# Optimization experiments

Hardware: AMD Instinct MI355X
Metric: run time of the kernel (lower is better)

The kernel has to match this reference:

```python
import jax, jax.numpy as jnp
import numpy as np

N, EMB, CHEB_K, H, DIN = 512, 10, 2, 64, 2
LSTM_H = 130


def _avwgcn(x, S_base, mask_t, node_emb, W_pool, b_pool):
    # x: [B,N,C], S_base: [N,N] softmax(relu(E E^T)), mask_t: [B,N,N]
    B = x.shape[0]
    S = S_base[None, :, :] * mask_t                      # [B,N,N]
    eye = jnp.broadcast_to(jnp.eye(N, dtype=x.dtype), (B, N, N))
    supports = [eye, S]
    for _ in range(2, CHEB_K):
        supports.append(2.0 * jnp.matmul(S, supports[-1]) - supports[-2])
    sup = jnp.stack(supports, axis=0)                    # [K,B,N,N]
    weights = jnp.einsum('nd,dkio->nkio', node_emb, W_pool)   # [N,K,I,O]
    bias = node_emb @ b_pool                             # [N,O]
    x_g = jnp.einsum('kbnm,bmc->bnkc', sup, x)           # [B,N,K,C]
    return jnp.einsum('bnki,nkio->bno', x_g, weights) + bias


def _encoder(entity, entity_mask, node_emb, gW, gb, uW, ub):
    # entity: [B,T,N,DIN]; returns last hidden state [B,N,H]
    B = entity.shape[0]
    S_base = jax.nn.softmax(jax.nn.relu(node_emb @ node_emb.T), axis=-1)
    x_seq = jnp.swapaxes(entity, 0, 1)                   # [T,B,N,DIN]
    m_seq = jnp.swapaxes(entity_mask, 0, 1)              # [T,B,N,N]

    def step(state, xm):
        x_t, m_t = xm
        ins = jnp.concatenate([x_t, state], axis=-1)     # [B,N,DIN+H]
        z_r = jax.nn.sigmoid(_avwgcn(ins, S_base, m_t, node_emb, gW, gb))
        z, r = z_r[..., :H], z_r[..., H:]
        cand = jnp.concatenate([x_t, z * state], axis=-1)
        hc = jnp.tanh(_avwgcn(cand, S_base, m_t, node_emb, uW, ub))
        h = r * state + (1.0 - r) * hc
        return h, None

    state0 = jnp.zeros((B, N, H), dtype=entity.dtype)
    state, _ = jax.lax.scan(step, state0, (x_seq, m_seq))
    return state                                         # [B,N,H]


def _lstm_layer(x_seq, Wih, Whh, bih, bhh):
    # x_seq: [T,B,in]; PyTorch gate order i,f,g,o
    B = x_seq.shape[1]
    Hh = LSTM_H

    def step(carry, xt):
        h, c = carry
        g = xt @ Wih.T + h @ Whh.T + bih + bhh           # [B,4H]
        i = jax.nn.sigmoid(g[:, :Hh])
        f = jax.nn.sigmoid(g[:, Hh:2 * Hh])
        gg = jnp.tanh(g[:, 2 * Hh:3 * Hh])
        o = jax.nn.sigmoid(g[:, 3 * Hh:])
        c = f * c + i * gg
        h = o * jnp.tanh(c)
        return (h, c), h

    init = (jnp.zeros((B, Hh), x_seq.dtype), jnp.zeros((B, Hh), x_seq.dtype))
    (_, _), hs = jax.lax.scan(step, init, x_seq)
    return hs                                            # [T,B,H]


def setup_inputs() -> dict:
    key = jax.random.key(0)
    ks = jax.random.split(key, 20)
    s = 0.1
    inp = {
        'entity': jax.random.normal(ks[0], (16, 12, N, DIN), jnp.float32),
        'entity_mask': jnp.ones((16, 12, N, N), jnp.float32),
        's_and_r': jax.random.normal(ks[1], (16, 32, 64), jnp.float32),
        'node_emb': jax.random.normal(ks[2], (N, EMB), jnp.float32),
        'gW': jax.random.normal(ks[3], (EMB, CHEB_K, DIN + H, 2 * H), jnp.float32) * s,
        'gb': jax.random.normal(ks[4], (EMB, 2 * H), jnp.float32) * s,
        'uW': jax.random.normal(ks[5], (EMB, CHEB_K, DIN + H, H), jnp.float32) * s,
        'ub': jax.random.normal(ks[6], (EMB, H), jnp.float32) * s,
        'lstm_Wih0': jax.random.normal(ks[7], (4 * LSTM_H, 64), jnp.float32) * s,
        'lstm_Whh0': jax.random.normal(ks[8], (4 * LSTM_H, LSTM_H), jnp.float32) * s,
        'lstm_bih0': jax.random.normal(ks[9], (4 * LSTM_H,), jnp.float32) * s,
        'lstm_bhh0': jax.random.normal(ks[10], (4 * LSTM_H,), jnp.float32) * s,
        'lstm_Wih1': jax.random.normal(ks[11], (4 * LSTM_H, LSTM_H), jnp.float32) * s,
        'lstm_Whh1': jax.random.normal(ks[12], (4 * LSTM_H, LSTM_H), jnp.float32) * s,
        'lstm_bih1': jax.random.normal(ks[13], (4 * LSTM_H,), jnp.float32) * s,
        'lstm_bhh1': jax.random.normal(ks[14], (4 * LSTM_H,), jnp.float32) * s,
        'fc_W': jax.random.normal(ks[15], (24, LSTM_H + H), jnp.float32) * s,
        'fc_b': jax.random.normal(ks[16], (24,), jnp.float32) * s,
    }
    return inp


def reference(entity, entity_mask, s_and_r, node_emb, gW, gb, uW, ub,
              lstm_Wih0, lstm_Whh0, lstm_bih0, lstm_bhh0,
              lstm_Wih1, lstm_Whh1, lstm_bih1, lstm_bhh1, fc_W, fc_b):
    B = entity.shape[0]
    # graph encoder: last hidden state, max over nodes
    h_graph = _encoder(entity, entity_mask, node_emb, gW, gb, uW, ub)  # [B,N,H]
    graph_out = jnp.max(h_graph, axis=1)                               # [B,H]
    # 2-layer LSTM (eval mode, dropout inactive)
    x_seq = jnp.swapaxes(s_and_r, 0, 1)                 # [T,B,in]
    h1 = _lstm_layer(x_seq, lstm_Wih0, lstm_Whh0, lstm_bih0, lstm_bhh0)
    h2 = _lstm_layer(h1, lstm_Wih1, lstm_Whh1, lstm_bih1, lstm_bhh1)
    sr_out = h2[-1]                                      # [B,130]
    feat = jnp.concatenate([sr_out, graph_out], axis=-1)
    out = jax.nn.sigmoid(feat @ fc_W.T + fc_b)           # [B,24]
    return out.reshape(B, 12, 2)
```

## Files before the change

### kernel.cpp

```cpp
#include <hip/hip_runtime.h>
#include <math.h>

#define NN 512
#define EMBD 10
#define HH 64
#define DINV 2
#define CIN 66
#define TT 12
#define BB 16
#define LH 130
#define LG 520
#define PART ((size_t)BB * NN * CIN)

typedef __attribute__((ext_vector_type(8))) short short8;
typedef __attribute__((ext_vector_type(8))) _Float16 half8;
typedef __attribute__((ext_vector_type(4))) float f32x4;
typedef __attribute__((ext_vector_type(2))) _Float16 h2v;

__device__ __forceinline__ float sigmoidf_(float x) { return 1.f / (1.f + __expf(-x)); }
__device__ __forceinline__ float tanhf_(float x)    { return 1.f - 2.f / (1.f + __expf(2.f * x)); }
__device__ __forceinline__ unsigned short f16u_(float v) {
    return __builtin_bit_cast(unsigned short, (_Float16)v);
}
__device__ __forceinline__ unsigned pkh_(float a, float b) {
    return (unsigned)f16u_(a) | ((unsigned)f16u_(b) << 16);
}
__device__ __forceinline__ float fdot2_(unsigned h, unsigned w, float c) {
#if __has_builtin(__builtin_amdgcn_fdot2)
    return __builtin_amdgcn_fdot2(__builtin_bit_cast(h2v, h), __builtin_bit_cast(h2v, w), c, false);
#else
    h2v H = __builtin_bit_cast(h2v, h), W = __builtin_bit_cast(h2v, w);
    return c + (float)H[0] * (float)W[0] + (float)H[1] * (float)W[1];
#endif
}
__device__ __forceinline__ float plo_(unsigned u) { return (float)__builtin_bit_cast(h2v, u)[0]; }
__device__ __forceinline__ float phi_(unsigned u) { return (float)__builtin_bit_cast(h2v, u)[1]; }
__device__ __forceinline__ half8 ld8h_(const unsigned short* p) {
    return __builtin_bit_cast(half8, *(const short8*)p);
}

__global__ __launch_bounds__(256) void precompute1_kernel(
    const float* __restrict__ emb, float* __restrict__ Sb,
    const float* __restrict__ gW, const float* __restrict__ uW,
    unsigned short* __restrict__ WgF, unsigned short* __restrict__ WuF,
    const float* __restrict__ gb, const float* __restrict__ ub,
    float* __restrict__ bgc, float* __restrict__ buc,
    const float* __restrict__ Wih0, const float* __restrict__ Whh0,
    const float* __restrict__ Wih1, const float* __restrict__ Whh1,
    unsigned* __restrict__ wp_ih0, unsigned* __restrict__ wp_hh0,
    unsigned* __restrict__ wp_ih1, unsigned* __restrict__ wp_hh1) {
    __shared__ float poolS[EMBD * 512];
    __shared__ float embS[128 * EMBD];
    __shared__ float redw[4];
    const int bid = blockIdx.x;
    const int tid = threadIdx.x;
    if (bid < 512) {
        const int n = bid;
        float* en = embS;
        if (tid < EMBD) en[tid] = emb[n * EMBD + tid];
        __syncthreads();
        float v[2];
        #pragma unroll
        for (int q = 0; q < 2; q++) {
            int m = tid + q * 256;
            float s = 0.f;
            #pragma unroll
            for (int d = 0; d < EMBD; d++) s += en[d] * emb[m * EMBD + d];
            v[q] = fmaxf(s, 0.f);
        }
        float mx = fmaxf(v[0], v[1]);
        for (int off = 32; off >= 1; off >>= 1) mx = fmaxf(mx, __shfl_xor(mx, off));
        if ((tid & 63) == 0) redw[tid >> 6] = mx;
        __syncthreads();
        mx = fmaxf(fmaxf(redw[0], redw[1]), fmaxf(redw[2], redw[3]));
        __syncthreads();
        v[0] = __expf(v[0] - mx);
        v[1] = __expf(v[1] - mx);
        float sm = v[0] + v[1];
        for (int off = 32; off >= 1; off >>= 1) sm += __shfl_xor(sm, off);
        if ((tid & 63) == 0) redw[tid >> 6] = sm;
        __syncthreads();
        sm = redw[0] + redw[1] + redw[2] + redw[3];
        float inv = 1.f / sm;
        Sb[n * NN + tid]       = v[0] * inv;
        Sb[n * NN + tid + 256] = v[1] * inv;
        return;
    }
    if (bid < 752) {
        const int bb = bid - 512;
        const int group = bb % 60;
        const int chunk = bb / 60;
        const float* pool;
        unsigned short* outU;
        int OT, Ow, ot, kc;
        if (group < 40) { pool = gW; outU = WgF; Ow = 128; OT = 8; ot = group / 5; kc = group % 5; }
        else { int g2 = group - 40; pool = uW; outU = WuF; Ow = 64; OT = 4; ot = g2 / 5; kc = g2 % 5; }
        for (int l = tid; l < EMBD * 512; l += 256) {
            int d = l >> 9, rem = l & 511;
            int kpl = rem >> 4, ol = rem & 15;
            int kp = kc * 32 + kpl;
            float v = 0.f;
            if (kp < 2 * CIN) v = pool[((size_t)d * (2 * CIN) + kp) * Ow + ot * 16 + ol];
            poolS[l] = v;
        }
        for (int l = tid; l < 128 * EMBD; l += 256) {
            int nl = l / EMBD, d = l - nl * EMBD;
            embS[l] = emb[(chunk * 128 + nl) * EMBD + d];
        }
        __syncthreads();
        const int e0 = tid * 2, e1 = e0 + 1;
        const int l0 = e0 >> 3, j0 = e0 & 7, p0 = (((l0 >> 4) << 3) + j0) * 16 + (l0 & 15);
        const int l1 = e1 >> 3, j1 = e1 & 7, p1 = (((l1 >> 4) << 3) + j1) * 16 + (l1 & 15);
        float w0[EMBD], w1[EMBD];
        #pragma unroll
        for (int d = 0; d < EMBD; d++) {
            w0[d] = poolS[d * 512 + p0];
            w1[d] = poolS[d * 512 + p1];
        }
        for (int nl = 0; nl < 128; nl++) {
            int n = chunk * 128 + nl;
            float a0 = 0.f, a1 = 0.f;
            #pragma unroll
            for (int d = 0; d < EMBD; d++) {
                float e = embS[nl * EMBD + d];
                a0 += e * w0[d];
                a1 += e * w1[d];
            }
            size_t base = (((size_t)n * OT + ot) * 5 + kc) * 512;
            *(unsigned*)(outU + base + e0) = pkh_(a0, a1);
        }
        return;
    }
    if (bid < 1136) {
        int idx = (bid - 752) * 256 + tid;
        if (idx < NN * 128) {
            int n = idx >> 7, rem = idx & 127;
            float a = 0.f;
            #pragma unroll
            for (int d = 0; d < EMBD; d++) a += emb[n * EMBD + d] * gb[d * 128 + rem];
            bgc[idx] = a;
        } else if (idx < NN * 128 + NN * 64) {
            int j = idx - NN * 128;
            int n = j >> 6, rem = j & 63;
            float a = 0.f;
            #pragma unroll
            for (int d = 0; d < EMBD; d++) a += emb[n * EMBD + d] * ub[d * 64 + rem];
            buc[j] = a;
        }
        return;
    }
    {
        int idx = (bid - 1136) * 256 + tid;
        const float* w;
        unsigned* wp;
        int K, base;
        if (idx < 16640)       { w = Wih0; wp = wp_ih0; K = 64;  base = 0; }
        else if (idx < 50440)  { w = Whh0; wp = wp_hh0; K = 130; base = 16640; }
        else if (idx < 84240)  { w = Wih1; wp = wp_ih1; K = 130; base = 50440; }
        else if (idx < 118040) { w = Whh1; wp = wp_hh1; K = 130; base = 84240; }
        else return;
        int j2 = idx - base;
        int kk = j2 / LG, j = j2 - kk * LG;
        wp[j2] = pkh_(w[j * K + 2 * kk], w[j * K + 2 * kk + 1]);
    }
}

__device__ void lstm_body(int b, int tid,
    const float* __restrict__ sr,
    const unsigned* __restrict__ wp_ih0, const float* __restrict__ Wih0,
    const float* __restrict__ bih0, const float* __restrict__ bhh0,
    const unsigned* __restrict__ wp_hh0, const float* __restrict__ Whh0,
    const unsigned* __restrict__ wp_ih1, const float* __restrict__ Wih1,
    const float* __restrict__ bih1, const float* __restrict__ bhh1,
    const unsigned* __restrict__ wp_hh1, const float* __restrict__ Whh1,
    float* __restrict__ h2last) {
    const int lane = tid & 63;
    const int wv = tid >> 6;
    __shared__ __align__(16) float xp[32 * 520];
    __shared__ __align__(16) unsigned h1p[32 * 68];
    __shared__ __align__(16) float h1s[32 * 132];
    __shared__ __align__(16) unsigned xsp[32 * 32];
    __shared__ __align__(16) unsigned hP[68];
    __shared__ __align__(16) float hS[132], cS[132];
    __shared__ float gS[520];
    __shared__ float WeX[130 * 8];
    unsigned wpk[65];

    for (int l = tid; l < 32 * 32; l += 512) {
        float2 v = *(const float2*)&sr[(size_t)b * 2048 + 2 * l];
        xsp[l] = pkh_(v.x, v.y);
    }
    #pragma unroll
    for (int kk = 0; kk < 32; kk++) wpk[kk] = wp_ih0[kk * 520 + tid];
    for (int l = tid; l < 64 * 8; l += 512) { int k = l >> 3, je = l & 7; WeX[l] = Wih0[(512 + je) * 64 + k]; }
    __syncthreads();
    {
        float bias = bih0[tid] + bhh0[tid];
        for (int t = 0; t < 32; t++) {
            const uint4* x4 = (const uint4*)&xsp[t * 32];
            float a0 = bias, a1 = 0.f;
            #pragma unroll
            for (int q = 0; q < 8; q++) {
                uint4 hq = x4[q];
                a0 = fdot2_(hq.x, wpk[4 * q + 0], a0);
                a1 = fdot2_(hq.y, wpk[4 * q + 1], a1);
                a0 = fdot2_(hq.z, wpk[4 * q + 2], a0);
                a1 = fdot2_(hq.w, wpk[4 * q + 3], a1);
            }
            xp[t * 520 + tid] = a0 + a1;
        }
        if (tid < 256) {
            int je = tid & 7, t = tid >> 3;
            float a = bih0[512 + je] + bhh0[512 + je];
            for (int p = 0; p < 32; p++) {
                unsigned u = xsp[t * 32 + p];
                a += plo_(u) * WeX[(2 * p) * 8 + je] + phi_(u) * WeX[(2 * p + 1) * 8 + je];
            }
            xp[t * 520 + 512 + je] = a;
        }
    }
    __syncthreads();

    #pragma unroll
    for (int kk = 0; kk < 65; kk++) wpk[kk] = wp_hh0[kk * 520 + tid];
    for (int l = tid; l < 130 * 8; l += 512) { int k = l >> 3, je = l & 7; WeX[l] = Whh0[(512 + je) * 130 + k]; }
    for (int l = tid; l < 132; l += 512) { hS[l] = 0.f; cS[l] = 0.f; }
    if (tid < 68) hP[tid] = 0u;
    __syncthreads();
    {
        float we0 = WeX[lane * 8 + wv];
        float we1 = WeX[(lane + 64) * 8 + wv];
        float we2 = (lane < 2) ? WeX[(lane + 128) * 8 + wv] : 0.f;
        for (int t = 0; t < 32; t++) {
            const uint4* hp4 = (const uint4*)hP;
            float a0 = xp[t * 520 + tid], a1 = 0.f;
            #pragma unroll
            for (int q = 0; q < 16; q++) {
                uint4 hq = hp4[q];
                a0 = fdot2_(hq.x, wpk[4 * q + 0], a0);
                a1 = fdot2_(hq.y, wpk[4 * q + 1], a1);
                a0 = fdot2_(hq.z, wpk[4 * q + 2], a0);
                a1 = fdot2_(hq.w, wpk[4 * q + 3], a1);
            }
            a0 = fdot2_(hP[64], wpk[64], a0);
            gS[tid] = a0 + a1;
            float p = hS[lane] * we0 + hS[lane + 64] * we1;
            if (lane < 2) p += hS[lane + 128] * we2;
            #pragma unroll
            for (int off = 32; off >= 1; off >>= 1) p += __shfl_xor(p, off);
            if (lane == 0) gS[512 + wv] = xp[t * 520 + 512 + wv] + p;
            __syncthreads();
            if (tid < 130) {
                float iv = sigmoidf_(gS[tid]);
                float fv = sigmoidf_(gS[130 + tid]);
                float gv = tanhf_(gS[260 + tid]);
                float ov = sigmoidf_(gS[390 + tid]);
                float cv = fv * cS[tid] + iv * gv;
                cS[tid] = cv;
                float hv = ov * tanhf_(cv);
                hS[tid] = hv;
                h1s[t * 132 + tid] = hv;
                float nb = __shfl_xor(hv, 1);
                if ((tid & 1) == 0) {
                    unsigned pk = pkh_(hv, nb);
                    hP[tid >> 1] = pk;
                    h1p[t * 68 + (tid >> 1)] = pk;
                }
            }
            __syncthreads();
        }
    }

    #pragma unroll
    for (int kk = 0; kk < 65; kk++) wpk[kk] = wp_ih1[kk * 520 + tid];
    for (int l = tid; l < 130 * 8; l += 512) { int k = l >> 3, je = l & 7; WeX[l] = Wih1[(512 + je) * 130 + k]; }
    __syncthreads();
    {
        float bias = bih1[tid] + bhh1[tid];
        for (int t = 0; t < 32; t++) {
            const uint4* x4 = (const uint4*)&h1p[t * 68];
            float a0 = bias, a1 = 0.f;
            #pragma unroll
            for (int q = 0; q < 16; q++) {
                uint4 hq = x4[q];
                a0 = fdot2_(hq.x, wpk[4 * q + 0], a0);
                a1 = fdot2_(hq.y, wpk[4 * q + 1], a1);
                a0 = fdot2_(hq.z, wpk[4 * q + 2], a0);
                a1 = fdot2_(hq.w, wpk[4 * q + 3], a1);
            }
            a0 = fdot2_(h1p[t * 68 + 64], wpk[64], a0);
            xp[t * 520 + tid] = a0 + a1;
        }
        if (tid < 256) {
            int je = tid & 7, t = tid >> 3;
            float a = bih1[512 + je] + bhh1[512 + je];
            for (int k = 0; k < 130; k++) a += h1s[t * 132 + k] * WeX[k * 8 + je];
            xp[t * 520 + 512 + je] = a;
        }
    }
    __syncthreads();

    #pragma unroll
    for (int kk = 0; kk < 65; kk++) wpk[kk] = wp_hh1[kk * 520 + tid];
    for (int l = tid; l < 130 * 8; l += 512) { int k = l >> 3, je = l & 7; WeX[l] = Whh1[(512 + je) * 130 + k]; }
    for (int l = tid; l < 132; l += 512) { hS[l] = 0.f; cS[l] = 0.f; }
    if (tid < 68) hP[tid] = 0u;
    __syncthreads();
    {
        float we0 = WeX[lane * 8 + wv];
        float we1 = WeX[(lane + 64) * 8 + wv];
        float we2 = (lane < 2) ? WeX[(lane + 128) * 8 + wv] : 0.f;
        for (int t = 0; t < 32; t++) {
            const uint4* hp4 = (const uint4*)hP;
            float a0 = xp[t * 520 + tid], a1 = 0.f;
            #pragma unroll
            for (int q = 0; q < 16; q++) {
                uint4 hq = hp4[q];
                a0 = fdot2_(hq.x, wpk[4 * q + 0], a0);
                a1 = fdot2_(hq.y, wpk[4 * q + 1], a1);
                a0 = fdot2_(hq.z, wpk[4 * q + 2], a0);
                a1 = fdot2_(hq.w, wpk[4 * q + 3], a1);
            }
            a0 = fdot2_(hP[64], wpk[64], a0);
            gS[tid] = a0 + a1;
            float p = hS[lane] * we0 + hS[lane + 64] * we1;
            if (lane < 2) p += hS[lane + 128] * we2;
            #pragma unroll
            for (int off = 32; off >= 1; off >>= 1) p += __shfl_xor(p, off);
            if (lane == 0) gS[512 + wv] = xp[t * 520 + 512 + wv] + p;
            __syncthreads();
            if (tid < 130) {
                float iv = sigmoidf_(gS[tid]);
                float fv = sigmoidf_(gS[130 + tid]);
                float gv = tanhf_(gS[260 + tid]);
                float ov = sigmoidf_(gS[390 + tid]);
                float cv = fv * cS[tid] + iv * gv;
                cS[tid] = cv;
                float hv = ov * tanhf_(cv);
                hS[tid] = hv;
                float nb = __shfl_xor(hv, 1);
                if ((tid & 1) == 0) hP[tid >> 1] = pkh_(hv, nb);
                if (t == 31) h2last[(size_t)b * LH + tid] = hv;
            }
            __syncthreads();
        }
    }
}

__global__ __launch_bounds__(512) void mega_kernel(
    const float* __restrict__ Sb, const float* __restrict__ mask,
    unsigned short* __restrict__ AF,
    const float* __restrict__ ent, unsigned short* __restrict__ Xf,
    float* __restrict__ state,
    const float* __restrict__ sr,
    const unsigned* __restrict__ wp_ih0, const float* __restrict__ Wih0,
    const float* __restrict__ bih0, const float* __restrict__ bhh0,
    const unsigned* __restrict__ wp_hh0, const float* __restrict__ Whh0,
    const unsigned* __restrict__ wp_ih1, const float* __restrict__ Wih1,
    const float* __restrict__ bih1, const float* __restrict__ bhh1,
    const unsigned* __restrict__ wp_hh1, const float* __restrict__ Whh1,
    float* __restrict__ h2last) {
    const int bid = blockIdx.x;
    const int tid = threadIdx.x;
    if (bid < 16) {
        lstm_body(bid, tid, sr, wp_ih0, Wih0, bih0, bhh0, wp_hh0, Whh0,
                  wp_ih1, Wih1, bih1, bhh1, wp_hh1, Whh1, h2last);
        return;
    }
    if (bid < 176) {
        int idx = (bid - 16) * 512 + tid;
        int l = idx & 63;
        int r = idx >> 6;
        int kc = r & 1; r >>= 1;
        int ct = r % 5; r /= 5;
        int q = r & 7;
        int b = r >> 3;
        const int c = ct * 16 + (l & 15);
        const int mbase = q * 64 + kc * 32 + ((l >> 4) & 3) * 8;
        union { unsigned short u[8]; short8 v; } o;
        #pragma unroll
        for (int j = 0; j < 8; j++) {
            int m = mbase + j;
            float v = 0.f;
            if (c < DINV) v = ent[((size_t)(b * TT + 0) * NN + m) * DINV + c];
            o.u[j] = f16u_(v);
        }
        size_t base = ((((size_t)b * 8 + q) * 5 + ct) * 2 + kc) * 512;
        *(short8*)(Xf + base + l * 8) = o.v;
        return;
    }
    if (bid < 1200) {
        int i = (bid - 176) * 512 + tid;
        state[i] = 0.f;
        return;
    }
    size_t idx = (size_t)(bid - 1200) * 512 + tid;
    int l = (int)(idx & 63);
    size_t f = idx >> 6;
    int mch = (int)(f & 15); f >>= 4;
    int ntile = (int)(f & 31); f >>= 5;
    int t = (int)(f % 12);
    int b = (int)(f / 12);
    int nrow = ntile * 16 + (l & 15);
    int m0 = mch * 32 + ((l >> 4) & 3) * 8;
    const float4* s4 = (const float4*)(Sb + (size_t)nrow * NN + m0);
    const float4* m4 = (const float4*)(mask + ((size_t)(b * TT + t) * NN + nrow) * NN + m0);
    float4 sa = s4[0], sc = s4[1];
    float4 ma = m4[0], mc = m4[1];
    union { unsigned short u[8]; short8 v; } o;
    o.u[0] = f16u_(sa.x * ma.x); o.u[1] = f16u_(sa.y * ma.y);
    o.u[2] = f16u_(sa.z * ma.z); o.u[3] = f16u_(sa.w * ma.w);
    o.u[4] = f16u_(sc.x * mc.x); o.u[5] = f16u_(sc.y * mc.y);
    o.u[6] = f16u_(sc.z * mc.z); o.u[7] = f16u_(sc.w * mc.w);
    *(short8*)(AF + idx * 8) = o.v;
}

__global__ __launch_bounds__(256) void spmm_kernel(const unsigned short* __restrict__ AF,
                                                   const unsigned short* __restrict__ Xf,
                                                   float* __restrict__ out, int t) {
    const int tid = threadIdx.x;
    const int lane = tid & 63;
    const int w = tid >> 6;
    const int b = blockIdx.y;
    const int z = blockIdx.z;
    float* __restrict__ outp = out + (size_t)z * PART;
    const int ntile = blockIdx.x * 4 + w;

    f32x4 acc[5];
    #pragma unroll
    for (int ct = 0; ct < 5; ct++) acc[ct] = (f32x4){0.f, 0.f, 0.f, 0.f};

    #pragma unroll
    for (int r2 = 0; r2 < 2; r2++) {
        #pragma unroll
        for (int kc = 0; kc < 2; kc++) {
            const int mch = z * 4 + r2 * 2 + kc;
            const int q = z * 2 + r2;
            half8 a = ld8h_(AF + ((((size_t)b * TT + t) * 32 + ntile) * 16 + mch) * 512 + lane * 8);
            #pragma unroll
            for (int ct = 0; ct < 5; ct++) {
                half8 bf = ld8h_(Xf + ((((size_t)b * 8 + q) * 5 + ct) * 2 + kc) * 512 + lane * 8);
                acc[ct] = __builtin_amdgcn_mfma_f32_16x16x32_f16(a, bf, acc[ct], 0, 0, 0);
            }
        }
    }
    const int col = lane & 15, rq = lane >> 4;
    #pragma unroll
    for (int ct = 0; ct < 5; ct++) {
        int c = ct * 16 + col;
        if (c < CIN) {
            #pragma unroll
            for (int reg = 0; reg < 4; reg++) {
                int n = ntile * 16 + rq * 4 + reg;
                outp[(size_t)b * NN * CIN + n * CIN + c] = acc[ct][reg];
            }
        }
    }
}

__global__ __launch_bounds__(256) void gate_mfma_kernel(const float* __restrict__ ent,
                                                        const float* __restrict__ state,
                                                        const float* __restrict__ xg1,
                                                        const unsigned short* __restrict__ WgF,
                                                        const float* __restrict__ bg,
                                                        float* __restrict__ cand,
                                                        float* __restrict__ rbuf,
                                                        unsigned short* __restrict__ Xf,
                                                        int t) {
    __shared__ unsigned short A_h[16 * 168];
    const int n = blockIdx.x;
    const int tid = threadIdx.x;
    const int lane = tid & 63;
    const int w = tid >> 6;
    for (int idx = tid; idx < 16 * 36; idx += 256) {
        int b = idx / 36, k = 132 + idx - b * 36;
        A_h[b * 168 + k] = 0;
    }
    for (int idx = tid; idx < 16 * 132; idx += 256) {
        int b = idx / 132, ip = idx - b * 132;
        float v;
        if (ip < CIN) {
            v = (ip < DINV) ? ent[((size_t)(b * TT + t) * NN + n) * DINV + ip]
                            : state[((size_t)b * NN + n) * HH + (ip - DINV)];
        } else {
            size_t g = (size_t)b * NN * CIN + n * CIN + (ip - CIN);
            v = xg1[g] + xg1[g + PART] + xg1[g + 2 * PART] + xg1[g + 3 * PART];
        }
        A_h[b * 168 + ip] = f16u_(v);
    }
    __syncthreads();

    f32x4 acc0 = {0.f, 0.f, 0.f, 0.f}, acc1 = {0.f, 0.f, 0.f, 0.f};
    const unsigned short* Wn = WgF + (size_t)n * (8 * 5 * 512);
    #pragma unroll
    for (int kc = 0; kc < 5; kc++) {
        int aoff = (lane & 15) * 168 + kc * 32 + (lane >> 4) * 8;
        half8 ah = ld8h_(&A_h[aoff]);
        half8 bh0 = ld8h_(Wn + ((size_t)(w * 5) + kc) * 512 + lane * 8);
        half8 bh1 = ld8h_(Wn + ((size_t)((w + 4) * 5) + kc) * 512 + lane * 8);
        acc0 = __builtin_amdgcn_mfma_f32_16x16x32_f16(ah, bh0, acc0, 0, 0, 0);
        acc1 = __builtin_amdgcn_mfma_f32_16x16x32_f16(ah, bh1, acc1, 0, 0, 0);
    }
    const int col = lane & 15, rq = lane >> 4;
    const int q = n >> 6, kcn = (n >> 5) & 1, jn = n & 7;
    {
        int o = w * 16 + col;
        int c = o + DINV;
        int ct = c >> 4, cl = c & 15;
        int l = ((n >> 3) & 3) * 16 + cl;
        float bias = bg[n * 128 + o];
        #pragma unroll
        for (int reg = 0; reg < 4; reg++) {
            int b = rq * 4 + reg;
            float zr = sigmoidf_(acc0[reg] + bias);
            float val = zr * state[((size_t)b * NN + n) * HH + o];
            cand[(size_t)b * NN * CIN + n * CIN + c] = val;
            size_t fb = ((((size_t)b * 8 + q) * 5 + ct) * 2 + kcn) * 512;
            Xf[fb + l * 8 + jn] = f16u_(val);
        }
    }
    {
        int o = (w + 4) * 16 + col;
        float bias = bg[n * 128 + o];
        #pragma unroll
        for (int reg = 0; reg < 4; reg++) {
            int b = rq * 4 + reg;
            float zr = sigmoidf_(acc1[reg] + bias);
            rbuf[((size_t)b * NN + n) * HH + (o - HH)] = zr;
        }
    }
    if (tid < 32) {
        int b = tid >> 1, i = tid & 1;
        cand[(size_t)b * NN * CIN + n * CIN + i] =
            ent[((size_t)(b * TT + t) * NN + n) * DINV + i];
    }
}

__global__ __launch_bounds__(256) void update_mfma_kernel(const float* __restrict__ cand,
                                                          const float* __restrict__ xg2,
                                                          const unsigned short* __restrict__ WuF,
                                                          const float* __restrict__ bu,
                                                          const float* __restrict__ rbuf,
                                                          float* __restrict__ state,
                                                          unsigned short* __restrict__ Xf,
                                                          const float* __restrict__ ent,
                                                          int tnext) {
    __shared__ unsigned short A_h[16 * 168];
    const int n = blockIdx.x;
    const int tid = threadIdx.x;
    const int lane = tid & 63;
    const int w = tid >> 6;
    for (int idx = tid; idx < 16 * 36; idx += 256) {
        int b = idx / 36, k = 132 + idx - b * 36;
        A_h[b * 168 + k] = 0;
    }
    for (int idx = tid; idx < 16 * 132; idx += 256) {
        int b = idx / 132, ip = idx - b * 132;
        float v;
        if (ip < CIN) {
            v = cand[(size_t)b * NN * CIN + n * CIN + ip];
        } else {
            size_t g = (size_t)b * NN * CIN + n * CIN + (ip - CIN);
            v = xg2[g] + xg2[g + PART] + xg2[g + 2 * PART] + xg2[g + 3 * PART];
        }
        A_h[b * 168 + ip] = f16u_(v);
    }
    __syncthreads();

    f32x4 acc = {0.f, 0.f, 0.f, 0.f};
    const unsigned short* Wn = WuF + (size_t)n * (4 * 5 * 512);
    #pragma unroll
    for (int kc = 0; kc < 5; kc++) {
        int aoff = (lane & 15) * 168 + kc * 32 + (lane >> 4) * 8;
        half8 ah = ld8h_(&A_h[aoff]);
        half8 bh = ld8h_(Wn + ((size_t)(w * 5) + kc) * 512 + lane * 8);
        acc = __builtin_amdgcn_mfma_f32_16x16x32_f16(ah, bh, acc, 0, 0, 0);
    }
    const int col = lane & 15, rq = lane >> 4;
    const int q = n >> 6, kcn = (n >> 5) & 1, jn = n & 7;
    int o = w * 16 + col;
    int c = o + DINV;
    int ct = c >> 4, cl = c & 15;
    int l = ((n >> 3) & 3) * 16 + cl;
    float bias = bu[n * HH + o];
    #pragma unroll
    for (int reg = 0; reg < 4; reg++) {
        int b = rq * 4 + reg;
        float hc = tanhf_(acc[reg] + bias);
        size_t g = ((size_t)b * NN + n) * HH + o;
        float rr = rbuf[g];
        float ns = rr * state[g] + (1.f - rr) * hc;
        state[g] = ns;
        size_t fb = ((((size_t)b * 8 + q) * 5 + ct) * 2 + kcn) * 512;
        Xf[fb + l * 8 + jn] = f16u_(ns);
    }
    if (w == 0 && col < DINV && tnext < TT) {
        int le = ((n >> 3) & 3) * 16 + col;
        #pragma unroll
        for (int reg = 0; reg < 4; reg++) {
            int b = rq * 4 + reg;
            float v = ent[((size_t)(b * TT + tnext) * NN + n) * DINV + col];
            size_t fb = ((((size_t)b * 8 + q) * 5 + 0) * 2 + kcn) * 512;
            Xf[fb + le * 8 + jn] = f16u_(v);
        }
    }
}

__global__ __launch_bounds__(256) void final_kernel(const float* __restrict__ state,
                                                    const float* __restrict__ h2last,
                                                    const float* __restrict__ fcW,
                                                    const float* __restrict__ fcb,
                                                    float* __restrict__ out) {
    const int b = blockIdx.x;
    const int tid = threadIdx.x;
    __shared__ float feat[LH + HH];
    __shared__ float red[4][HH];
    const int hh = tid & 63, q = tid >> 6;
    float mx = -INFINITY;
    for (int n = q * 128; n < q * 128 + 128; n++)
        mx = fmaxf(mx, state[((size_t)b * NN + n) * HH + hh]);
    red[q][hh] = mx;
    if (tid >= 64 && tid < 64 + LH)
        feat[tid - 64] = h2last[(size_t)b * LH + (tid - 64)];
    __syncthreads();
    if (tid < HH)
        feat[LH + tid] = fmaxf(fmaxf(red[0][tid], red[1][tid]), fmaxf(red[2][tid], red[3][tid]));
    __syncthreads();
    if (tid < 24) {
        float a = fcb[tid];
        for (int k = 0; k < LH + HH; k++) a += feat[k] * fcW[tid * (LH + HH) + k];
        out[b * 24 + tid] = sigmoidf_(a);
    }
}

extern "C" void kernel_launch(void* const* d_in, const int* in_sizes, int n_in,
                              void* d_out, int out_size, void* d_ws, size_t ws_size,
                              hipStream_t stream) {
    const float* ent  = (const float*)d_in[0];
    const float* mask = (const float*)d_in[1];
    const float* sr   = (const float*)d_in[2];
    const float* emb  = (const float*)d_in[3];
    const float* gW   = (const float*)d_in[4];
    const float* gb   = (const float*)d_in[5];
    const float* uW   = (const float*)d_in[6];
    const float* ub   = (const float*)d_in[7];
    const float* Wih0 = (const float*)d_in[8];
    const float* Whh0 = (const float*)d_in[9];
    const float* bih0 = (const float*)d_in[10];
    const float* bhh0 = (const float*)d_in[11];
    const float* Wih1 = (const float*)d_in[12];
    const float* Whh1 = (const float*)d_in[13];
    const float* bih1 = (const float*)d_in[14];
    const float* bhh1 = (const float*)d_in[15];
    const float* fcW  = (const float*)d_in[16];
    const float* fcb  = (const float*)d_in[17];
    float* out = (float*)d_out;
    float* ws = (float*)d_ws;

    size_t off = 0;
    float* Sb     = ws + off; off += (size_t)NN * NN;
    unsigned short* WgF = (unsigned short*)(ws + off); off += (size_t)NN * 8 * 5 * 256;
    unsigned short* WuF = (unsigned short*)(ws + off); off += (size_t)NN * 4 * 5 * 256;
    unsigned short* AF  = (unsigned short*)(ws + off); off += (size_t)BB * TT * 32 * 16 * 256;
    float* bgc    = ws + off; off += (size_t)NN * 128;
    float* buc    = ws + off; off += (size_t)NN * HH;
    float* state  = ws + off; off += (size_t)BB * NN * HH;
    float* xgP    = ws + off; off += 4 * PART;
    float* cand   = ws + off; off += PART;
    float* rbuf   = ws + off; off += (size_t)BB * NN * HH;
    float* h2last = ws + off; off += (size_t)BB * LH;
    unsigned short* Xf = (unsigned short*)(ws + off); off += (size_t)BB * 8 * 5 * 2 * 256;
    unsigned* wp_ih0 = (unsigned*)(ws + off); off += 32 * LG;
    unsigned* wp_hh0 = (unsigned*)(ws + off); off += 65 * LG;
    unsigned* wp_ih1 = (unsigned*)(ws + off); off += 65 * LG;
    unsigned* wp_hh1 = (unsigned*)(ws + off); off += 65 * LG;

    precompute1_kernel<<<1598, 256, 0, stream>>>(emb, Sb, gW, uW, WgF, WuF, gb, ub, bgc, buc,
                                                 Wih0, Whh0, Wih1, Whh1,
                                                 wp_ih0, wp_hh0, wp_ih1, wp_hh1);
    mega_kernel<<<13488, 512, 0, stream>>>(Sb, mask, AF, ent, Xf, state, sr,
                                           wp_ih0, Wih0, bih0, bhh0, wp_hh0, Whh0,
                                           wp_ih1, Wih1, bih1, bhh1, wp_hh1, Whh1, h2last);

    for (int t = 0; t < TT; t++) {
        spmm_kernel<<<dim3(8, BB, 4), 256, 0, stream>>>(AF, Xf, xgP, t);
        gate_mfma_kernel<<<NN, 256, 0, stream>>>(ent, state, xgP, WgF, bgc, cand, rbuf, Xf, t);
        spmm_kernel<<<dim3(8, BB, 4), 256, 0, stream>>>(AF, Xf, xgP, t);
        update_mfma_kernel<<<NN, 256, 0, stream>>>(cand, xgP, WuF, buc, rbuf, state, Xf, ent, t + 1);
    }

    final_kernel<<<BB, 256, 0, stream>>>(state, h2last, fcW, fcb, out);
}
```

Measured before the change: 643.2 us.

## Interleave LSTM recurrent gate rows so each quad computes its cell update

```diff
diff --git a/kernel.cpp b/kernel.cpp
--- a/kernel.cpp
+++ b/kernel.cpp
@@ -153,15 +153,20 @@
         int idx = (bid - 1136) * 256 + tid;
         const float* w;
         unsigned* wp;
-        int K, base;
-        if (idx < 16640)       { w = Wih0; wp = wp_ih0; K = 64;  base = 0; }
-        else if (idx < 50440)  { w = Whh0; wp = wp_hh0; K = 130; base = 16640; }
-        else if (idx < 84240)  { w = Wih1; wp = wp_ih1; K = 130; base = 50440; }
-        else if (idx < 118040) { w = Whh1; wp = wp_hh1; K = 130; base = 84240; }
+        int K, base, hh;
+        if (idx < 16640)       { w = Wih0; wp = wp_ih0; K = 64;  base = 0;     hh = 0; }
+        else if (idx < 50440)  { w = Whh0; wp = wp_hh0; K = 130; base = 16640; hh = 1; }
+        else if (idx < 84240)  { w = Wih1; wp = wp_ih1; K = 130; base = 50440; hh = 0; }
+        else if (idx < 118040) { w = Whh1; wp = wp_hh1; K = 130; base = 84240; hh = 1; }
         else return;
         int j2 = idx - base;
         int kk = j2 / LG, j = j2 - kk * LG;
-        wp[j2] = pkh_(w[j * K + 2 * kk], w[j * K + 2 * kk + 1]);
+        int dst = j;
+        if (hh) {
+            int u = j % 130, gg = j / 130;
+            dst = (u < 128) ? (u * 4 + gg) : (512 + (u - 128) * 4 + gg);
+        }
+        wp[kk * LG + dst] = pkh_(w[j * K + 2 * kk], w[j * K + 2 * kk + 1]);
     }
 }
 
@@ -174,17 +179,17 @@
     const float* __restrict__ bih1, const float* __restrict__ bhh1,
     const unsigned* __restrict__ wp_hh1, const float* __restrict__ Whh1,
     float* __restrict__ h2last) {
-    const int lane = tid & 63;
-    const int wv = tid >> 6;
     __shared__ __align__(16) float xp[32 * 520];
-    __shared__ __align__(16) unsigned h1p[32 * 68];
-    __shared__ __align__(16) float h1s[32 * 132];
+    __shared__ __align__(16) unsigned short h1ph[32 * 136];
     __shared__ __align__(16) unsigned xsp[32 * 32];
-    __shared__ __align__(16) unsigned hP[68];
-    __shared__ __align__(16) float hS[132], cS[132];
-    __shared__ float gS[520];
+    __shared__ __align__(16) unsigned short hPh[2][136];
+    __shared__ __align__(16) unsigned WeH[8 * 66];
     __shared__ float WeX[130 * 8];
     unsigned wpk[65];
+    const int g = tid & 3, ju = tid >> 2;
+    const int xrow = g * 130 + ju;
+    const int lw = tid & 63;
+    const bool w0 = (tid < 64);
 
     for (int l = tid; l < 32 * 32; l += 512) {
         float2 v = *(const float2*)&sr[(size_t)b * 2048 + 2 * l];
@@ -223,48 +228,69 @@
 
     #pragma unroll
     for (int kk = 0; kk < 65; kk++) wpk[kk] = wp_hh0[kk * 520 + tid];
-    for (int l = tid; l < 130 * 8; l += 512) { int k = l >> 3, je = l & 7; WeX[l] = Whh0[(512 + je) * 130 + k]; }
-    for (int l = tid; l < 132; l += 512) { hS[l] = 0.f; cS[l] = 0.f; }
-    if (tid < 68) hP[tid] = 0u;
+    for (int l = tid; l < 8 * 65; l += 512) {
+        int rw = l / 65, kp = l - rw * 65;
+        WeH[rw * 66 + kp] = wp_hh0[kp * 520 + 512 + rw];
+    }
+    for (int l = tid; l < 2 * 136; l += 512) ((unsigned short*)hPh)[l] = 0;
     __syncthreads();
     {
-        float we0 = WeX[lane * 8 + wv];
-        float we1 = WeX[(lane + 64) * 8 + wv];
-        float we2 = (lane < 2) ? WeX[(lane + 128) * 8 + wv] : 0.f;
+        float creg = 0.f, cx = 0.f;
         for (int t = 0; t < 32; t++) {
-            const uint4* hp4 = (const uint4*)hP;
-            float a0 = xp[t * 520 + tid], a1 = 0.f;
+            const unsigned short* hc = hPh[t & 1];
+            unsigned short* hn = hPh[(t + 1) & 1];
+            const uint4* h4 = (const uint4*)hc;
+            float a0 = xp[t * 520 + xrow], a1 = 0.f;
             #pragma unroll
             for (int q = 0; q < 16; q++) {
-                uint4 hq = hp4[q];
+                uint4 hq = h4[q];
                 a0 = fdot2_(hq.x, wpk[4 * q + 0], a0);
                 a1 = fdot2_(hq.y, wpk[4 * q + 1], a1);
                 a0 = fdot2_(hq.z, wpk[4 * q + 2], a0);
                 a1 = fdot2_(hq.w, wpk[4 * q + 3], a1);
             }
-            a0 = fdot2_(hP[64], wpk[64], a0);
-            gS[tid] = a0 + a1;
-            float p = hS[lane] * we0 + hS[lane + 64] * we1;
-            if (lane < 2) p += hS[lane + 128] * we2;
-            #pragma unroll
-            for (int off = 32; off >= 1; off >>= 1) p += __shfl_xor(p, off);
-            if (lane == 0) gS[512 + wv] = xp[t * 520 + 512 + wv] + p;
-            __syncthreads();
-            if (tid < 130) {
-                float iv = sigmoidf_(gS[tid]);
-                float fv = sigmoidf_(gS[130 + tid]);
-                float gv = tanhf_(gS[260 + tid]);
-                float ov = sigmoidf_(gS[390 + tid]);
-                float cv = fv * cS[tid] + iv * gv;
-                cS[tid] = cv;
-                float hv = ov * tanhf_(cv);
-                hS[tid] = hv;
-                h1s[t * 132 + tid] = hv;
-                float nb = __shfl_xor(hv, 1);
-                if ((tid & 1) == 0) {
-                    unsigned pk = pkh_(hv, nb);
-                    hP[tid >> 1] = pk;
-                    h1p[t * 68 + (tid >> 1)] = pk;
+            a0 = fdot2_(*(const unsigned*)(hc + 128), wpk[64], a0);
+            float p = a0 + a1;
+            float p1 = __shfl_xor(p, 1);
+            float p2 = __shfl_xor(p, 2);
+            float p3 = __shfl_xor(p1, 2);
+            float ip = (g == 0) ? p : (g == 1) ? p1 : (g == 2) ? p2 : p3;
+            float fp = (g == 1) ? p : (g == 0) ? p1 : (g == 3) ? p2 : p3;
+            float gp = (g == 2) ? p : (g == 3) ? p1 : (g == 0) ? p2 : p3;
+            float op = (g == 3) ? p : (g == 2) ? p1 : (g == 1) ? p2 : p3;
+            float iv = sigmoidf_(ip), fv = sigmoidf_(fp), gv = tanhf_(gp), ov = sigmoidf_(op);
+            float cv = fv * creg + iv * gv;
+            creg = cv;
+            float hv = ov * tanhf_(cv);
+            if (g == 0) {
+                unsigned short hu = f16u_(hv);
+                hn[ju] = hu;
+                h1ph[t * 136 + ju] = hu;
+            }
+            if (w0) {
+                int rw = lw >> 3;
+                float e0 = 0.f;
+                for (int kp = (lw & 7); kp < 65; kp += 8)
+                    e0 = fdot2_(*(const unsigned*)(hc + 2 * kp), WeH[rw * 66 + kp], e0);
+                e0 += __shfl_xor(e0, 1);
+                e0 += __shfl_xor(e0, 2);
+                e0 += __shfl_xor(e0, 4);
+                int er = (rw & 3) * 130 + 128 + (rw >> 2);
+                float pe = e0 + xp[t * 520 + er];
+                int bl = lw & 32;
+                float pi_ = __shfl(pe, bl);
+                float pf_ = __shfl(pe, bl + 8);
+                float pg_ = __shfl(pe, bl + 16);
+                float po_ = __shfl(pe, bl + 24);
+                if ((lw & 31) == 0) {
+                    float iv2 = sigmoidf_(pi_), fv2 = sigmoidf_(pf_), gv2 = tanhf_(pg_), ov2 = sigmoidf_(po_);
+                    float cv2 = fv2 * cx + iv2 * gv2;
+                    cx = cv2;
+                    float hv2 = ov2 * tanhf_(cv2);
+                    int uu = 128 + (lw >> 5);
+                    unsigned short hu2 = f16u_(hv2);
+                    hn[uu] = hu2;
+                    h1ph[t * 136 + uu] = hu2;
                 }
             }
             __syncthreads();
@@ -278,7 +304,7 @@
     {
         float bias = bih1[tid] + bhh1[tid];
         for (int t = 0; t < 32; t++) {
-            const uint4* x4 = (const uint4*)&h1p[t * 68];
+            const uint4* x4 = (const uint4*)&h1ph[t * 136];
             float a0 = bias, a1 = 0.f;
             #pragma unroll
             for (int q = 0; q < 16; q++) {
@@ -288,13 +314,16 @@
                 a0 = fdot2_(hq.z, wpk[4 * q + 2], a0);
                 a1 = fdot2_(hq.w, wpk[4 * q + 3], a1);
             }
-            a0 = fdot2_(h1p[t * 68 + 64], wpk[64], a0);
+            a0 = fdot2_(*(const unsigned*)&h1ph[t * 136 + 128], wpk[64], a0);
             xp[t * 520 + tid] = a0 + a1;
         }
         if (tid < 256) {
             int je = tid & 7, t = tid >> 3;
             float a = bih1[512 + je] + bhh1[512 + je];
-            for (int k = 0; k < 130; k++) a += h1s[t * 132 + k] * WeX[k * 8 + je];
+            for (int k = 0; k < 65; k++) {
+                unsigned u = *(const unsigned*)&h1ph[t * 136 + 2 * k];
+                a += plo_(u) * WeX[(2 * k) * 8 + je] + phi_(u) * WeX[(2 * k + 1) * 8 + je];
+            }
             xp[t * 520 + 512 + je] = a;
         }
     }
@@ -302,45 +331,68 @@
 
     #pragma unroll
     for (int kk = 0; kk < 65; kk++) wpk[kk] = wp_hh1[kk * 520 + tid];
-    for (int l = tid; l < 130 * 8; l += 512) { int k = l >> 3, je = l & 7; WeX[l] = Whh1[(512 + je) * 130 + k]; }
-    for (int l = tid; l < 132; l += 512) { hS[l] = 0.f; cS[l] = 0.f; }
-    if (tid < 68) hP[tid] = 0u;
+    for (int l = tid; l < 8 * 65; l += 512) {
+        int rw = l / 65, kp = l - rw * 65;
+        WeH[rw * 66 + kp] = wp_hh1[kp * 520 + 512 + rw];
+    }
+    for (int l = tid; l < 2 * 136; l += 512) ((unsigned short*)hPh)[l] = 0;
     __syncthreads();
     {
-        float we0 = WeX[lane * 8 + wv];
-        float we1 = WeX[(lane + 64) * 8 + wv];
-        float we2 = (lane < 2) ? WeX[(lane + 128) * 8 + wv] : 0.f;
+        float creg = 0.f, cx = 0.f;
         for (int t = 0; t < 32; t++) {
-            const uint4* hp4 = (const uint4*)hP;
-            float a0 = xp[t * 520 + tid], a1 = 0.f;
+            const unsigned short* hc = hPh[t & 1];
+            unsigned short* hn = hPh[(t + 1) & 1];
+            const uint4* h4 = (const uint4*)hc;
+            float a0 = xp[t * 520 + xrow], a1 = 0.f;
             #pragma unroll
             for (int q = 0; q < 16; q++) {
-                uint4 hq = hp4[q];
+                uint4 hq = h4[q];
                 a0 = fdot2_(hq.x, wpk[4 * q + 0], a0);
                 a1 = fdot2_(hq.y, wpk[4 * q + 1], a1);
                 a0 = fdot2_(hq.z, wpk[4 * q + 2], a0);
                 a1 = fdot2_(hq.w, wpk[4 * q + 3], a1);
             }
-            a0 = fdot2_(hP[64], wpk[64], a0);
-            gS[tid] = a0 + a1;
-            float p = hS[lane] * we0 + hS[lane + 64] * we1;
-            if (lane < 2) p += hS[lane + 128] * we2;
-            #pragma unroll
-            for (int off = 32; off >= 1; off >>= 1) p += __shfl_xor(p, off);
-            if (lane == 0) gS[512 + wv] = xp[t * 520 + 512 + wv] + p;
-            __syncthreads();
-            if (tid < 130) {
-                float iv = sigmoidf_(gS[tid]);
-                float fv = sigmoidf_(gS[130 + tid]);
-                float gv = tanhf_(gS[260 + tid]);
-                float ov = sigmoidf_(gS[390 + tid]);
-                float cv = fv * cS[tid] + iv * gv;
-                cS[tid] = cv;
-                float hv = ov * tanhf_(cv);
-                hS[tid] = hv;
-                float nb = __shfl_xor(hv, 1);
-                if ((tid & 1) == 0) hP[tid >> 1] = pkh_(hv, nb);
-                if (t == 31) h2last[(size_t)b * LH + tid] = hv;
+            a0 = fdot2_(*(const unsigned*)(hc + 128), wpk[64], a0);
+            float p = a0 + a1;
+            float p1 = __shfl_xor(p, 1);
+            float p2 = __shfl_xor(p, 2);
+            float p3 = __shfl_xor(p1, 2);
+            float ip = (g == 0) ? p : (g == 1) ? p1 : (g == 2) ? p2 : p3;
+            float fp = (g == 1) ? p : (g == 0) ? p1 : (g == 3) ? p2 : p3;
+            float gp = (g == 2) ? p : (g == 3) ? p1 : (g == 0) ? p2 : p3;
+            float op = (g == 3) ? p : (g == 2) ? p1 : (g == 1) ? p2 : p3;
+            float iv = sigmoidf_(ip), fv = sigmoidf_(fp), gv = tanhf_(gp), ov = sigmoidf_(op);
+            float cv = fv * creg + iv * gv;
+            creg = cv;
+            float hv = ov * tanhf_(cv);
+            if (g == 0) {
+                hn[ju] = f16u_(hv);
+                if (t == 31) h2last[(size_t)b * LH + ju] = hv;
+            }
+            if (w0) {
+                int rw = lw >> 3;
+                float e0 = 0.f;
+                for (int kp = (lw & 7); kp < 65; kp += 8)
+                    e0 = fdot2_(*(const unsigned*)(hc + 2 * kp), WeH[rw * 66 + kp], e0);
+                e0 += __shfl_xor(e0, 1);
+                e0 += __shfl_xor(e0, 2);
+                e0 += __shfl_xor(e0, 4);
+                int er = (rw & 3) * 130 + 128 + (rw >> 2);
+                float pe = e0 + xp[t * 520 + er];
+                int bl = lw & 32;
+                float pi_ = __shfl(pe, bl);
+                float pf_ = __shfl(pe, bl + 8);
+                float pg_ = __shfl(pe, bl + 16);
+                float po_ = __shfl(pe, bl + 24);
+                if ((lw & 31) == 0) {
+                    float iv2 = sigmoidf_(pi_), fv2 = sigmoidf_(pf_), gv2 = tanhf_(pg_), ov2 = sigmoidf_(po_);
+                    float cv2 = fv2 * cx + iv2 * gv2;
+                    cx = cv2;
+                    float hv2 = ov2 * tanhf_(cv2);
+                    int uu = 128 + (lw >> 5);
+                    hn[uu] = f16u_(hv2);
+                    if (t == 31) h2last[(size_t)b * LH + uu] = hv2;
+                }
             }
             __syncthreads();
         }
```

New measurement: 653.8 us. Within noise of the previous version (+1.7%).
